# Kernel tuning notes

Hardware: AMD Instinct MI355X
Metric: run time of the kernel (lower is better)

Reference implementation:

```python
import jax, jax.numpy as jnp
import numpy as np

EPS = 1e-6
NH, D_NOPE, D_ROPE, DV = 16, 128, 64, 128
DQK = D_NOPE + D_ROPE  # 192
KV_LORA = 512
Q_LORA = 1536
TOP_K, N_GROUP, TOPK_GROUP, N_EXP = 2, 4, 2, 8
INTER = 768
SCALING = DQK ** -0.5  # rope_scaling is None -> no yarn mscale
RSF = 2.5  # routed_scaling_factor


def rms_norm(x, w):
    v = jnp.mean(jnp.square(x), axis=-1, keepdims=True)
    return x * jax.lax.rsqrt(v + EPS) * w


def rotate_half(x):
    x1, x2 = jnp.split(x, 2, axis=-1)
    return jnp.concatenate([-x2, x1], axis=-1)


def interleave(x):
    # view(b,h,s,d//2,2).transpose(4,3).reshape(b,h,s,d): evens then odds
    b, h, s, d = x.shape
    return x.reshape(b, h, s, d // 2, 2).swapaxes(-1, -2).reshape(b, h, s, d)


def mlp(x, gw, uw, dw):
    return (jax.nn.silu(x @ gw.T) * (x @ uw.T)) @ dw.T


def setup_inputs() -> dict:
    key = jax.random.key(0)
    ks = jax.random.split(key, 16)
    B, S, H = 2, 1024, 2048
    sd = 0.02

    def p(k, shape):
        return jax.random.normal(k, shape, jnp.float32) * sd

    # standard RoPE cos/sin table
    inv_freq = 1.0 / (10000.0 ** (jnp.arange(0, D_ROPE, 2, dtype=jnp.float32) / D_ROPE))
    pos = jnp.arange(S, dtype=jnp.float32)
    freqs = pos[:, None] * inv_freq[None, :]
    emb = jnp.concatenate([freqs, freqs], axis=-1)  # [S, D_ROPE]
    cos = jnp.broadcast_to(jnp.cos(emb)[None], (B, S, D_ROPE))
    sin = jnp.broadcast_to(jnp.sin(emb)[None], (B, S, D_ROPE))

    return dict(
        hidden_states=jax.random.normal(ks[0], (B, S, H), jnp.float32),
        cos=cos,
        sin=sin,
        ln1_w=jnp.ones((H,), jnp.float32),
        q_a_w=p(ks[1], (Q_LORA, H)),
        q_a_ln_w=jnp.ones((Q_LORA,), jnp.float32),
        q_b_w=p(ks[2], (NH * DQK, Q_LORA)),
        kv_a_w=p(ks[3], (KV_LORA + D_ROPE, H)),
        kv_a_ln_w=jnp.ones((KV_LORA,), jnp.float32),
        kv_b_w=p(ks[4], (NH * (D_NOPE + DV), KV_LORA)),
        o_w=p(ks[5], (H, NH * DV)),
        ln2_w=jnp.ones((H,), jnp.float32),
        router_w=p(ks[6], (N_EXP, H)),
        router_bias=jnp.zeros((N_EXP,), jnp.float32),
        gate_w=p(ks[7], (N_EXP, INTER, H)),
        up_w=p(ks[8], (N_EXP, INTER, H)),
        down_w=p(ks[9], (N_EXP, H, INTER)),
        sh_gate_w=p(ks[10], (INTER, H)),
        sh_up_w=p(ks[11], (INTER, H)),
        sh_down_w=p(ks[12], (H, INTER)),
    )


def reference(hidden_states, cos, sin, ln1_w, q_a_w, q_a_ln_w, q_b_w, kv_a_w,
              kv_a_ln_w, kv_b_w, o_w, ln2_w, router_w, router_bias,
              gate_w, up_w, down_w, sh_gate_w, sh_up_w, sh_down_w):
    B, S, H = hidden_states.shape
    # ----- input_layernorm + MLA attention -----
    resid = hidden_states
    x = rms_norm(hidden_states, ln1_w)

    q = rms_norm(x @ q_a_w.T, q_a_ln_w) @ q_b_w.T       # [B,S,NH*DQK]
    q = q.reshape(B, S, NH, DQK).transpose(0, 2, 1, 3)   # [B,NH,S,DQK]
    q_pass, q_rot = q[..., :D_NOPE], q[..., D_NOPE:]

    ckv = x @ kv_a_w.T                                   # [B,S,KV_LORA+D_ROPE]
    k_pass_c, k_rot = ckv[..., :KV_LORA], ckv[..., KV_LORA:]
    kv = rms_norm(k_pass_c, kv_a_ln_w) @ kv_b_w.T        # [B,S,NH*(D_NOPE+DV)]
    kv = kv.reshape(B, S, NH, D_NOPE + DV).transpose(0, 2, 1, 3)
    k_pass, v = kv[..., :D_NOPE], kv[..., D_NOPE:]

    k_rot = k_rot.reshape(B, 1, S, D_ROPE)
    c = cos[:, None]  # [B,1,S,D_ROPE]
    s_ = sin[:, None]
    q_rot = interleave(q_rot)
    k_rot = interleave(k_rot)
    q_rot = q_rot * c + rotate_half(q_rot) * s_
    k_rot = k_rot * c + rotate_half(k_rot) * s_
    k_rot = jnp.broadcast_to(k_rot, (B, NH, S, D_ROPE))

    qs = jnp.concatenate([q_pass, q_rot], axis=-1)       # [B,NH,S,DQK]
    ks = jnp.concatenate([k_pass, k_rot], axis=-1)

    scores = jnp.einsum('bhqd,bhkd->bhqk', qs, ks) * SCALING
    causal = jnp.tril(jnp.ones((S, S), dtype=bool))
    scores = jnp.where(causal, scores, -jnp.inf)
    probs = jax.nn.softmax(scores, axis=-1)
    attn = jnp.einsum('bhqk,bhkd->bhqd', probs, v)
    attn = attn.transpose(0, 2, 1, 3).reshape(B, S, NH * DV)
    x = resid + attn @ o_w.T

    # ----- post_attention_layernorm + MoE -----
    resid = x
    h = rms_norm(x, ln2_w)
    t = h.reshape(-1, H)

    # router (fp32)
    scores_r = jax.nn.sigmoid(t.astype(jnp.float32) @ router_w.T.astype(jnp.float32))
    sc = scores_r + router_bias[None, :]
    gs = sc.reshape(-1, N_GROUP, N_EXP // N_GROUP)
    group_scores = jax.lax.top_k(gs, 2)[0].sum(-1)          # [T,G]
    gidx = jax.lax.top_k(group_scores, TOPK_GROUP)[1]
    gmask = jax.nn.one_hot(gidx, N_GROUP).sum(1)            # [T,G]
    emask = jnp.repeat(gmask, N_EXP // N_GROUP, axis=-1)    # [T,E]
    masked = jnp.where(emask > 0, sc, 0.0)
    idx = jax.lax.top_k(masked, TOP_K)[1]                   # [T,k]
    w = jnp.take_along_axis(scores_r, idx, axis=-1)
    w = w / (w.sum(-1, keepdims=True) + 1e-20) * RSF

    # routed experts: dense-all-experts compute, then routed-weight combine
    gate_h = jnp.einsum('td,eid->tei', t, gate_w)
    up_h = jnp.einsum('td,eid->tei', t, up_w)
    eo = jnp.einsum('tei,edi->ted', jax.nn.silu(gate_h) * up_h, down_w)
    dense_w = (jax.nn.one_hot(idx, N_EXP) * w[..., None]).sum(1)  # [T,E]
    moe_out = jnp.einsum('ted,te->td', eo, dense_w).reshape(B, S, H)

    shared = mlp(h, sh_gate_w, sh_up_w, sh_down_w)
    return resid + moe_out + shared
```

## Files before the change

kernel.cpp:

```cpp
#include <hip/hip_runtime.h>

typedef float f4 __attribute__((ext_vector_type(4)));
typedef float f32x4 __attribute__((ext_vector_type(4)));
typedef unsigned short us8 __attribute__((ext_vector_type(8)));
typedef __bf16 bf8 __attribute__((ext_vector_type(8)));

static constexpr int B_ = 2, S_ = 1024, H_ = 2048, T_ = B_ * S_;
static constexpr int NH_ = 16, DN_ = 128, DR_ = 64, DV_ = 128, DQK_ = 192;
static constexpr int KVL_ = 512, QL_ = 1536, INTER_ = 768, NEXP_ = 8, NE9_ = 9;
static constexpr int QKA_ = 2176;
static constexpr float SCALING_ = 0.07216878364870322f;
static constexpr float EPS_ = 1e-6f;

__device__ __forceinline__ unsigned short f2bf(float f) {
    unsigned u = __float_as_uint(f);
    u += 0x7fffu + ((u >> 16) & 1u);
    return (unsigned short)(u >> 16);
}
__device__ __forceinline__ float bf2f(unsigned short h) {
    return __uint_as_float(((unsigned)h) << 16);
}
__device__ __forceinline__ us8 pack8(f4 a, f4 b) {
    us8 r;
    r[0] = f2bf(a[0]); r[1] = f2bf(a[1]); r[2] = f2bf(a[2]); r[3] = f2bf(a[3]);
    r[4] = f2bf(b[0]); r[5] = f2bf(b[1]); r[6] = f2bf(b[2]); r[7] = f2bf(b[3]);
    return r;
}

__device__ __forceinline__ void gload16(const unsigned short* g, unsigned short* lds) {
    __builtin_amdgcn_global_load_lds(
        (const __attribute__((address_space(1))) void*)g,
        (__attribute__((address_space(3))) void*)lds, 16, 0, 0);
}

template <int MODE>
__global__ __launch_bounds__(256) void gemm2(
    const unsigned short* __restrict__ A, const unsigned short* __restrict__ Bw,
    float* __restrict__ Cf, unsigned short* __restrict__ Cb,
    const float* __restrict__ add,
    const int* __restrict__ cnt, const int* __restrict__ off,
    const int* __restrict__ idxl, const float* __restrict__ wl,
    int M, int N, int K, int ldA, long sB)
{
    constexpr int BM = 128, BN = 128, BK = 32;
    __shared__ __align__(16) unsigned short As[5][BM * BK];
    __shared__ __align__(16) unsigned short Bs[5][BN * BK];
    const int tid = threadIdx.x, lane = tid & 63, wv = tid >> 6;
    const int wm = (wv >> 1) * 64, wn = (wv & 1) * 64;

    const int nb = gridDim.x * gridDim.y;
    const int lin = blockIdx.y * gridDim.x + blockIdx.x;
    const int swz = (lin & 7) * (nb >> 3) + (lin >> 3);
    const int bx = swz % gridDim.x;
    const int by = swz / gridDim.x;
    const int m0 = bx * BM, n0 = by * BN;

    int mcnt = M, obase = 0;
    if constexpr (MODE != 0) {
        mcnt = cnt[blockIdx.z];
        if (m0 >= mcnt) return;
        obase = off[blockIdx.z];
    }

    const int srow = tid >> 2, scol = (tid & 3) * 8;
    long aoff0, aoff1;
    if constexpr (MODE == 1) {
        const int e = blockIdx.z;
        int r0 = m0 + srow, r1 = r0 + 64;
        int t0 = idxl[(long)e * T_ + (r0 < mcnt ? r0 : mcnt - 1)];
        int t1 = idxl[(long)e * T_ + (r1 < mcnt ? r1 : mcnt - 1)];
        aoff0 = (long)t0 * ldA + scol;
        aoff1 = (long)t1 * ldA + scol;
    } else if constexpr (MODE == 2) {
        aoff0 = (long)(obase + m0 + srow) * ldA + scol;
        aoff1 = aoff0 + 64L * ldA;
    } else {
        aoff0 = (long)(m0 + srow) * ldA + scol;
        aoff1 = aoff0 + 64L * ldA;
    }
    long boff0 = (long)blockIdx.z * sB + (long)(n0 + srow) * K + scol;
    long boff1 = boff0 + 64L * K;

    f32x4 acc[4][4];
#pragma unroll
    for (int m = 0; m < 4; m++)
#pragma unroll
        for (int n = 0; n < 4; n++) acc[m][n] = f32x4{0.f, 0.f, 0.f, 0.f};

    const int fr = lane & 15, ko = (lane >> 4) * 8;

    auto stage = [&](int buf, int k0) {
        gload16(A + aoff0 + k0, &As[buf][wv * 512]);
        gload16(A + aoff1 + k0, &As[buf][2048 + wv * 512]);
        gload16(Bw + boff0 + k0, &Bs[buf][wv * 512]);
        gload16(Bw + boff1 + k0, &Bs[buf][2048 + wv * 512]);
    };
    auto compute = [&](int buf) {
        __builtin_amdgcn_s_setprio(1);
        bf8 af[4], bfv[4];
#pragma unroll
        for (int m = 0; m < 4; m++) af[m] = *(const bf8*)&As[buf][(wm + m * 16 + fr) * 32 + ko];
#pragma unroll
        for (int n = 0; n < 4; n++) bfv[n] = *(const bf8*)&Bs[buf][(wn + n * 16 + fr) * 32 + ko];
#pragma unroll
        for (int m = 0; m < 4; m++)
#pragma unroll
            for (int n = 0; n < 4; n++)
                acc[m][n] = __builtin_amdgcn_mfma_f32_16x16x32_bf16(af[m], bfv[n], acc[m][n], 0, 0, 0);
        __builtin_amdgcn_s_setprio(0);
    };

    const int nt = K / BK;
    stage(0, 0);
    stage(1, BK);
    stage(2, 2 * BK);
    stage(3, 3 * BK);
    for (int t = 0; t < nt; t++) {
        if (t + 3 < nt)      asm volatile("s_waitcnt vmcnt(12)" ::: "memory");
        else if (t + 2 < nt) asm volatile("s_waitcnt vmcnt(8)" ::: "memory");
        else if (t + 1 < nt) asm volatile("s_waitcnt vmcnt(4)" ::: "memory");
        else                 asm volatile("s_waitcnt vmcnt(0)" ::: "memory");
        __builtin_amdgcn_s_barrier();
        if (t + 4 < nt) stage((t + 4) % 5, (t + 4) * BK);
        compute(t % 5);
    }

#pragma unroll
    for (int m = 0; m < 4; m++) {
#pragma unroll
        for (int n = 0; n < 4; n++) {
#pragma unroll
            for (int i = 0; i < 4; i++) {
                int row = wm + m * 16 + (lane >> 4) * 4 + i;
                int col = n0 + wn + n * 16 + (lane & 15);
                float v = acc[m][n][i];
                if constexpr (MODE == 0) {
                    long idx = (long)(m0 + row) * N + col;
                    if (Cb)       Cb[idx] = f2bf(v);
                    else if (add) Cf[idx] = v + add[idx];
                    else          Cf[idx] = v;
                } else if constexpr (MODE == 1) {
                    if (m0 + row < mcnt)
                        Cb[(long)(obase + m0 + row) * N + col] = f2bf(v);
                } else {
                    if (m0 + row < mcnt) {
                        int e = blockIdx.z;
                        int tok = idxl[(long)e * T_ + m0 + row];
                        float w = wl[(long)e * T_ + m0 + row];
                        atomicAdd(&Cf[(long)tok * N + col], w * v);
                    }
                }
            }
        }
    }
}

__global__ __launch_bounds__(256) void fa_k(
    const unsigned short* __restrict__ qs, const unsigned short* __restrict__ ks,
    const unsigned short* __restrict__ vt, unsigned short* __restrict__ ab)
{
    constexpr int KB = 64;
    const int q0 = blockIdx.x * 64;
    const int bh = blockIdx.y;
    const int b = bh >> 4, h = bh & 15;
    const int tid = threadIdx.x, lane = tid & 63, wv = tid >> 6;
    const int fr = lane & 15, lg = lane >> 4;
    const int ko = lg * 8;

    __shared__ __align__(16) unsigned short Kl[KB][200];
    __shared__ __align__(16) unsigned short Vl[128][72];
    __shared__ __align__(16) unsigned short Pl[4][16][72];

    const unsigned short* qp = qs + ((long)bh * S_ + q0 + wv * 16 + fr) * DQK_ + ko;
    bf8 qf[6];
#pragma unroll
    for (int s = 0; s < 6; s++) qf[s] = *(const bf8*)(qp + s * 32);

    f32x4 o[8];
#pragma unroll
    for (int n = 0; n < 8; n++) o[n] = f32x4{0.f, 0.f, 0.f, 0.f};
    float mrow[4] = {-3e38f, -3e38f, -3e38f, -3e38f};
    float lrow[4] = {0.f, 0.f, 0.f, 0.f};

    const int nt = q0 / KB + 1;

    const unsigned short* kg = ks + ((long)bh * S_ + (tid >> 2)) * DQK_ + (tid & 3) * 48;
    const unsigned short* vg = vt + ((long)bh * DV_ + (tid >> 1)) * S_ + (tid & 1) * 32;

    us8 krg[6], vrg[4];
#pragma unroll
    for (int j = 0; j < 6; j++) krg[j] = *(const us8*)(kg + j * 8);
#pragma unroll
    for (int j = 0; j < 4; j++) vrg[j] = *(const us8*)(vg + j * 8);

    for (int t = 0; t < nt; t++) {
        __syncthreads();
        {
            int r = tid >> 2, c = (tid & 3) * 48;
#pragma unroll
            for (int j = 0; j < 6; j++) *(us8*)&Kl[r][c + j * 8] = krg[j];
            int dv = tid >> 1, c2 = (tid & 1) * 32;
#pragma unroll
            for (int j = 0; j < 4; j++) *(us8*)&Vl[dv][c2 + j * 8] = vrg[j];
        }
        __syncthreads();
        if (t + 1 < nt) {
            long kof = (long)(t + 1) * KB;
#pragma unroll
            for (int j = 0; j < 6; j++) krg[j] = *(const us8*)(kg + kof * DQK_ + j * 8);
#pragma unroll
            for (int j = 0; j < 4; j++) vrg[j] = *(const us8*)(vg + kof + j * 8);
        }
        f32x4 ps[4];
#pragma unroll
        for (int ct = 0; ct < 4; ct++) {
            f32x4 a = f32x4{0.f, 0.f, 0.f, 0.f};
#pragma unroll
            for (int s = 0; s < 6; s++) {
                bf8 kf = *(const bf8*)&Kl[ct * 16 + fr][s * 32 + ko];
                a = __builtin_amdgcn_mfma_f32_16x16x32_bf16(qf[s], kf, a, 0, 0, 0);
            }
            ps[ct] = a;
        }
        const int kv0 = t * KB;
        const bool diag = (kv0 == q0);
#pragma unroll
        for (int ct = 0; ct < 4; ct++)
#pragma unroll
            for (int i = 0; i < 4; i++) {
                float v = ps[ct][i] * SCALING_;
                if (diag && (kv0 + ct * 16 + fr) > (q0 + wv * 16 + lg * 4 + i)) v = -3e38f;
                ps[ct][i] = v;
            }
        float scl[4];
#pragma unroll
        for (int i = 0; i < 4; i++) {
            float v = fmaxf(fmaxf(ps[0][i], ps[1][i]), fmaxf(ps[2][i], ps[3][i]));
#pragma unroll
            for (int x = 8; x; x >>= 1) v = fmaxf(v, __shfl_xor(v, x, 16));
            float mn = fmaxf(mrow[i], v);
            scl[i] = __expf(mrow[i] - mn);
            mrow[i] = mn;
        }
        float tsum[4] = {0.f, 0.f, 0.f, 0.f};
#pragma unroll
        for (int ct = 0; ct < 4; ct++)
#pragma unroll
            for (int i = 0; i < 4; i++) {
                float e = __expf(ps[ct][i] - mrow[i]);
                tsum[i] += e;
                Pl[wv][lg * 4 + i][ct * 16 + fr] = f2bf(e);
            }
#pragma unroll
        for (int i = 0; i < 4; i++) {
            float v = tsum[i];
#pragma unroll
            for (int x = 8; x; x >>= 1) v += __shfl_xor(v, x, 16);
            lrow[i] = lrow[i] * scl[i] + v;
        }
#pragma unroll
        for (int n = 0; n < 8; n++)
#pragma unroll
            for (int i = 0; i < 4; i++) o[n][i] *= scl[i];
        bf8 pf[2];
#pragma unroll
        for (int ksl = 0; ksl < 2; ksl++)
            pf[ksl] = *(const bf8*)&Pl[wv][fr][ksl * 32 + ko];
#pragma unroll
        for (int n = 0; n < 8; n++)
#pragma unroll
            for (int ksl = 0; ksl < 2; ksl++) {
                bf8 vf = *(const bf8*)&Vl[n * 16 + fr][ksl * 32 + ko];
                o[n] = __builtin_amdgcn_mfma_f32_16x16x32_bf16(pf[ksl], vf, o[n], 0, 0, 0);
            }
    }
#pragma unroll
    for (int i = 0; i < 4; i++) {
        float inv = 1.f / lrow[i];
        long rbase = ((long)b * S_ + q0 + wv * 16 + lg * 4 + i) * H_ + h * DV_;
#pragma unroll
        for (int n = 0; n < 8; n++)
            ab[rbase + n * 16 + fr] = f2bf(o[n][i] * inv);
    }
}

__global__ __launch_bounds__(256) void cvt_k(
    const float* __restrict__ s, unsigned short* __restrict__ d, long n)
{
    long i = ((long)blockIdx.x * 256 + threadIdx.x) * 8;
    if (i < n) {
        f4 a = *(const f4*)(s + i);
        f4 b = *(const f4*)(s + i + 4);
        *(us8*)(d + i) = pack8(a, b);
    }
}

__global__ __launch_bounds__(256) void cvt_qka_k(
    const float* __restrict__ qa, const float* __restrict__ kva,
    unsigned short* __restrict__ d)
{
    long i = ((long)blockIdx.x * 256 + threadIdx.x) * 8;
    long row = i >> 11, col = i & 2047;
    us8 o;
    if (row < QL_) {
        const float* s = qa + row * H_ + col;
        o = pack8(*(const f4*)s, *(const f4*)(s + 4));
    } else if (row < QL_ + 576) {
        const float* s = kva + (row - QL_) * H_ + col;
        o = pack8(*(const f4*)s, *(const f4*)(s + 4));
    } else {
        o = us8{0, 0, 0, 0, 0, 0, 0, 0};
    }
    *(us8*)(d + i) = o;
}

__global__ __launch_bounds__(256) void cvt_cat9_k(
    const float* __restrict__ g, const float* __restrict__ u,
    const float* __restrict__ sg, const float* __restrict__ su,
    unsigned short* __restrict__ d)
{
    long ii = ((long)blockIdx.x * 256 + threadIdx.x) * 8;
    int e = blockIdx.y;
    long row = ii >> 11, col = ii & 2047;
    const float* src;
    if (row < INTER_)
        src = (e < 8) ? (g + ((long)e * INTER_ + row) * H_ + col) : (sg + row * H_ + col);
    else
        src = (e < 8) ? (u + ((long)e * INTER_ + row - INTER_) * H_ + col)
                      : (su + (row - INTER_) * H_ + col);
    *(us8*)(d + (long)e * (2 * INTER_) * H_ + ii) = pack8(*(const f4*)src, *(const f4*)(src + 4));
}

__global__ __launch_bounds__(256) void rmsnorm_f2b(
    const float* __restrict__ in, const float* __restrict__ w,
    unsigned short* __restrict__ ob, float* __restrict__ of)
{
    const long base = (long)blockIdx.x * H_;
    const int c = threadIdx.x * 8;
    f4 v0 = *(const f4*)(in + base + c);
    f4 v1 = *(const f4*)(in + base + c + 4);
    float ss = v0[0] * v0[0] + v0[1] * v0[1] + v0[2] * v0[2] + v0[3] * v0[3]
             + v1[0] * v1[0] + v1[1] * v1[1] + v1[2] * v1[2] + v1[3] * v1[3];
#pragma unroll
    for (int o = 32; o; o >>= 1) ss += __shfl_down(ss, o);
    __shared__ float red[4];
    if ((threadIdx.x & 63) == 0) red[threadIdx.x >> 6] = ss;
    __syncthreads();
    float r = rsqrtf((red[0] + red[1] + red[2] + red[3]) / H_ + EPS_);
    f4 w0 = *(const f4*)(w + c);
    f4 w1 = *(const f4*)(w + c + 4);
    f4 a, b;
#pragma unroll
    for (int j = 0; j < 4; j++) { a[j] = v0[j] * r * w0[j]; b[j] = v1[j] * r * w1[j]; }
    *(us8*)(ob + base + c) = pack8(a, b);
    if (of) {
        *(f4*)(of + base + c) = a;
        *(f4*)(of + base + c + 4) = b;
    }
}

__global__ __launch_bounds__(256) void rmsnorm_b2b(
    const unsigned short* __restrict__ in, const float* __restrict__ w,
    unsigned short* __restrict__ out, int cols, int istride, int ostride)
{
    const long ib = (long)blockIdx.x * istride;
    const long ob = (long)blockIdx.x * ostride;
    const int nu = cols >> 3;
    float ss = 0.f;
    for (int u = threadIdx.x; u < nu; u += 256) {
        us8 v = *(const us8*)(in + ib + u * 8);
#pragma unroll
        for (int j = 0; j < 8; j++) { float f = bf2f(v[j]); ss += f * f; }
    }
#pragma unroll
    for (int o = 32; o; o >>= 1) ss += __shfl_down(ss, o);
    __shared__ float red[4];
    if ((threadIdx.x & 63) == 0) red[threadIdx.x >> 6] = ss;
    __syncthreads();
    float r = rsqrtf((red[0] + red[1] + red[2] + red[3]) / cols + EPS_);
    for (int u = threadIdx.x; u < nu; u += 256) {
        us8 v = *(const us8*)(in + ib + u * 8);
        f4 w0 = *(const f4*)(w + u * 8);
        f4 w1 = *(const f4*)(w + u * 8 + 4);
        us8 o;
#pragma unroll
        for (int j = 0; j < 4; j++) o[j] = f2bf(bf2f(v[j]) * r * w0[j]);
#pragma unroll
        for (int j = 0; j < 4; j++) o[4 + j] = f2bf(bf2f(v[4 + j]) * r * w1[j]);
        *(us8*)(out + ob + u * 8) = o;
    }
}

__global__ __launch_bounds__(64) void rope_q_k(
    const unsigned short* __restrict__ q, const float* __restrict__ cs,
    const float* __restrict__ sn, unsigned short* __restrict__ qs)
{
    int t = blockIdx.x;
    int h = t & 15;
    int bs = t >> 4;
    int s = bs & (S_ - 1);
    int b = bs >> 10;
    const unsigned short* qrow = q + (long)bs * (NH_ * DQK_) + h * DQK_;
    unsigned short* orow = qs + ((long)(b * NH_ + h) * S_ + s) * DQK_;
    int l = threadIdx.x;
    orow[l] = qrow[l];
    orow[l + 64] = qrow[l + 64];
    int j = l & 31;
    float x0 = bf2f(qrow[DN_ + 2 * j]), x1 = bf2f(qrow[DN_ + 2 * j + 1]);
    float c = cs[(long)bs * DR_ + j], si = sn[(long)bs * DR_ + j];
    if (l < 32) orow[DN_ + j] = f2bf(x0 * c - x1 * si);
    else        orow[DN_ + 32 + j] = f2bf(x1 * c + x0 * si);
}

__global__ __launch_bounds__(64) void rope_k_k(
    const unsigned short* __restrict__ qkab, const float* __restrict__ cs,
    const float* __restrict__ sn, unsigned short* __restrict__ ks)
{
    int bs = blockIdx.x;
    int s = bs & (S_ - 1);
    int b = bs >> 10;
    const unsigned short* kr = qkab + (long)bs * QKA_ + QL_ + KVL_;
    int l = threadIdx.x;
    int j = l & 31;
    float x0 = bf2f(kr[2 * j]), x1 = bf2f(kr[2 * j + 1]);
    float c = cs[(long)bs * DR_ + j], si = sn[(long)bs * DR_ + j];
    float val = (l < 32) ? (x0 * c - x1 * si) : (x1 * c + x0 * si);
    int off = (l < 32) ? (DN_ + j) : (DN_ + 32 + j);
    unsigned short bv = f2bf(val);
    for (int h = 0; h < NH_; h++)
        ks[((long)(b * NH_ + h) * S_ + s) * DQK_ + off] = bv;
}

__global__ __launch_bounds__(128) void kpass_k(
    const unsigned short* __restrict__ kv, unsigned short* __restrict__ ks)
{
    int t = blockIdx.x;
    int h = t & 15;
    int bs = t >> 4;
    int s = bs & (S_ - 1);
    int b = bs >> 10;
    ks[((long)(b * NH_ + h) * S_ + s) * DQK_ + threadIdx.x] = kv[(long)t * 256 + threadIdx.x];
}

__global__ __launch_bounds__(256) void vt_k(
    const unsigned short* __restrict__ kv, unsigned short* __restrict__ vt)
{
    __shared__ unsigned short tile[64][DV_ + 8];
    int s0 = blockIdx.x * 64;
    int bh = blockIdx.y;
    int b = bh >> 4, h = bh & 15;
#pragma unroll
    for (int it = 0; it < 4; it++) {
        int idx = it * 256 + threadIdx.x;
        int sl = idx >> 4, du = idx & 15;
        *(us8*)&tile[sl][du * 8] =
            *(const us8*)(kv + ((long)(b * S_ + s0 + sl) * NH_ + h) * 256 + DN_ + du * 8);
    }
    __syncthreads();
#pragma unroll
    for (int it = 0; it < 4; it++) {
        int idx = it * 256 + threadIdx.x;
        int d = idx >> 3, su = idx & 7;
        us8 o;
#pragma unroll
        for (int j = 0; j < 8; j++) o[j] = tile[su * 8 + j][d];
        *(us8*)(vt + ((long)bh * DV_ + d) * S_ + s0 + su * 8) = o;
    }
}

__global__ void zero9_k(int* __restrict__ cnt)
{
    if (threadIdx.x < NE9_) cnt[threadIdx.x] = (threadIdx.x == 8) ? T_ : 0;
}

__global__ void offs_k(const int* __restrict__ cnt, int* __restrict__ off)
{
    if (threadIdx.x == 0) {
        int a = 0;
        for (int e = 0; e < NE9_; e++) { off[e] = a; a += cnt[e]; }
    }
}

__global__ __launch_bounds__(64) void router_k(
    const float* __restrict__ h, const float* __restrict__ rw,
    const float* __restrict__ rb, int* __restrict__ cnt,
    int* __restrict__ idxl, float* __restrict__ wl)
{
    int t = blockIdx.x;
    int l = threadIdx.x;
    const float* hr = h + (long)t * H_;
    float pe[8] = {0, 0, 0, 0, 0, 0, 0, 0};
    for (int k = l; k < H_; k += 64) {
        float hv = hr[k];
#pragma unroll
        for (int e = 0; e < 8; e++) pe[e] += hv * rw[e * H_ + k];
    }
#pragma unroll
    for (int e = 0; e < 8; e++)
        for (int o = 32; o; o >>= 1) pe[e] += __shfl_down(pe[e], o);
    if (l == 0) {
        float sr[8], sc[8];
#pragma unroll
        for (int e = 0; e < 8; e++) {
            sr[e] = 1.f / (1.f + __expf(-pe[e]));
            sc[e] = sr[e] + rb[e];
        }
        float gs[4];
        for (int g = 0; g < 4; g++) gs[g] = sc[2 * g] + sc[2 * g + 1];
        int g0 = 0;
        for (int g = 1; g < 4; g++) if (gs[g] > gs[g0]) g0 = g;
        int g1 = -1;
        for (int g = 0; g < 4; g++) {
            if (g == g0) continue;
            if (g1 < 0 || gs[g] > gs[g1]) g1 = g;
        }
        int i0 = -1, i1 = -1;
        for (int e = 0; e < 8; e++) {
            int g = e >> 1;
            if (g != g0 && g != g1) continue;
            if (i0 < 0 || sc[e] > sc[i0]) i0 = e;
        }
        for (int e = 0; e < 8; e++) {
            int g = e >> 1;
            if (g != g0 && g != g1) continue;
            if (e == i0) continue;
            if (i1 < 0 || sc[e] > sc[i1]) i1 = e;
        }
        float w0 = sr[i0], w1 = sr[i1];
        float inv = 2.5f / (w0 + w1 + 1e-20f);
        int p0 = atomicAdd(&cnt[i0], 1);
        idxl[i0 * T_ + p0] = t;
        wl[i0 * T_ + p0] = w0 * inv;
        int p1 = atomicAdd(&cnt[i1], 1);
        idxl[i1 * T_ + p1] = t;
        wl[i1 * T_ + p1] = w1 * inv;
        idxl[8 * T_ + t] = t;
        wl[8 * T_ + t] = 1.0f;
    }
}

__global__ __launch_bounds__(256) void silugu_k(
    const unsigned short* __restrict__ gu, unsigned short* __restrict__ act)
{
    long idx = (long)blockIdx.x * 256 + threadIdx.x;
    int r = (int)(idx / 96);
    int c = (int)(idx - (long)r * 96) * 8;
    us8 g8 = *(const us8*)(gu + (long)r * (2 * INTER_) + c);
    us8 u8 = *(const us8*)(gu + (long)r * (2 * INTER_) + INTER_ + c);
    us8 o;
#pragma unroll
    for (int j = 0; j < 8; j++) {
        float g = bf2f(g8[j]);
        o[j] = f2bf(g / (1.f + __expf(-g)) * bf2f(u8[j]));
    }
    *(us8*)(act + (long)r * INTER_ + c) = o;
}

extern "C" void kernel_launch(void* const* d_in, const int* in_sizes, int n_in,
                              void* d_out, int out_size, void* d_ws, size_t ws_size,
                              hipStream_t stream)
{
    const float* hidden = (const float*)d_in[0];
    const float* cosb   = (const float*)d_in[1];
    const float* sinb   = (const float*)d_in[2];
    const float* ln1w   = (const float*)d_in[3];
    const float* qaw    = (const float*)d_in[4];
    const float* qalnw  = (const float*)d_in[5];
    const float* qbw    = (const float*)d_in[6];
    const float* kvaw   = (const float*)d_in[7];
    const float* kvalnw = (const float*)d_in[8];
    const float* kvbw   = (const float*)d_in[9];
    const float* ow     = (const float*)d_in[10];
    const float* ln2w   = (const float*)d_in[11];
    const float* rw     = (const float*)d_in[12];
    const float* rb     = (const float*)d_in[13];
    const float* gw     = (const float*)d_in[14];
    const float* uw     = (const float*)d_in[15];
    const float* dwn    = (const float*)d_in[16];
    const float* sgw    = (const float*)d_in[17];
    const float* suw    = (const float*)d_in[18];
    const float* sdw    = (const float*)d_in[19];
    float* out = (float*)d_out;
    (void)in_sizes; (void)n_in; (void)out_size; (void)ws_size;

    char* ws = (char*)d_ws;
    const size_t MB = 1u << 20;
    unsigned short* qkawb = (unsigned short*)(ws + 0 * MB);
    unsigned short* qbwb  = (unsigned short*)(ws + 9 * MB);
    unsigned short* kvbwb = (unsigned short*)(ws + 18 * MB);
    unsigned short* owb   = (unsigned short*)(ws + 22 * MB);
    unsigned short* xb    = (unsigned short*)(ws + 30 * MB);
    unsigned short* qkab  = (unsigned short*)(ws + 38 * MB);
    unsigned short* qb16  = (unsigned short*)(ws + 47 * MB);
    unsigned short* ckvnb = (unsigned short*)(ws + 59 * MB);
    unsigned short* kvb   = (unsigned short*)(ws + 61 * MB);
    unsigned short* qs    = (unsigned short*)(ws + 77 * MB);
    unsigned short* ks    = (unsigned short*)(ws + 89 * MB);
    unsigned short* vt    = (unsigned short*)(ws + 30 * MB);
    unsigned short* ab    = (unsigned short*)(ws + 38 * MB);
    float* hbuf = (float*)(ws + 0 * MB);
    unsigned short* actm = (unsigned short*)(ws + 0 * MB);
    unsigned short* hb16 = (unsigned short*)(ws + 16 * MB);
    int*   cnt  = (int*)(ws + 24 * MB);
    int*   offb = (int*)(ws + 24 * MB + 256);
    int*   idxl = (int*)(ws + 24 * MB + 512);
    float* wl   = (float*)(ws + 24 * MB + 512 + 9 * T_ * 4);
    unsigned short* guwb = (unsigned short*)(ws + 25 * MB);
    unsigned short* dwnb = (unsigned short*)(ws + 25 * MB);
    unsigned short* gu   = (unsigned short*)(ws + 79 * MB);

    cvt_qka_k<<<(QKA_ * H_) / 2048, 256, 0, stream>>>(qaw, kvaw, qkawb);
    cvt_k<<<(NH_ * DQK_ * QL_) / 2048, 256, 0, stream>>>(qbw, qbwb, (long)NH_ * DQK_ * QL_);
    cvt_k<<<(NH_ * 256 * KVL_) / 2048, 256, 0, stream>>>(kvbw, kvbwb, (long)NH_ * 256 * KVL_);
    cvt_k<<<(H_ * H_) / 2048, 256, 0, stream>>>(ow, owb, (long)H_ * H_);

    rmsnorm_f2b<<<T_, 256, 0, stream>>>(hidden, ln1w, xb, nullptr);

    gemm2<0><<<dim3(T_ / 128, QKA_ / 128, 1), 256, 0, stream>>>(
        xb, qkawb, nullptr, qkab, nullptr, nullptr, nullptr, nullptr, nullptr,
        T_, QKA_, H_, H_, 0);
    rmsnorm_b2b<<<T_, 256, 0, stream>>>(qkab, qalnw, qkab, QL_, QKA_, QKA_);
    gemm2<0><<<dim3(T_ / 128, (NH_ * DQK_) / 128, 1), 256, 0, stream>>>(
        qkab, qbwb, nullptr, qb16, nullptr, nullptr, nullptr, nullptr, nullptr,
        T_, NH_ * DQK_, QL_, QKA_, 0);
    rmsnorm_b2b<<<T_, 256, 0, stream>>>(qkab + QL_, kvalnw, ckvnb, KVL_, QKA_, KVL_);
    gemm2<0><<<dim3(T_ / 128, (NH_ * 256) / 128, 1), 256, 0, stream>>>(
        ckvnb, kvbwb, nullptr, kvb, nullptr, nullptr, nullptr, nullptr, nullptr,
        T_, NH_ * 256, KVL_, KVL_, 0);

    rope_q_k<<<T_ * NH_, 64, 0, stream>>>(qb16, cosb, sinb, qs);
    rope_k_k<<<T_, 64, 0, stream>>>(qkab, cosb, sinb, ks);
    kpass_k<<<T_ * NH_, 128, 0, stream>>>(kvb, ks);
    vt_k<<<dim3(S_ / 64, B_ * NH_), 256, 0, stream>>>(kvb, vt);

    fa_k<<<dim3(S_ / 64, B_ * NH_), 256, 0, stream>>>(qs, ks, vt, ab);

    gemm2<0><<<dim3(T_ / 128, H_ / 128, 1), 256, 0, stream>>>(
        ab, owb, out, nullptr, hidden, nullptr, nullptr, nullptr, nullptr,
        T_, H_, H_, H_, 0);

    rmsnorm_f2b<<<T_, 256, 0, stream>>>(out, ln2w, hb16, hbuf);
    zero9_k<<<1, 64, 0, stream>>>(cnt);
    router_k<<<T_, 64, 0, stream>>>(hbuf, rw, rb, cnt, idxl, wl);
    offs_k<<<1, 64, 0, stream>>>(cnt, offb);

    cvt_cat9_k<<<dim3((2 * INTER_ * H_) / 2048, NE9_), 256, 0, stream>>>(gw, uw, sgw, suw, guwb);
    gemm2<1><<<dim3(T_ / 128, (2 * INTER_) / 128, NE9_), 256, 0, stream>>>(
        hb16, guwb, nullptr, gu, nullptr, cnt, offb, idxl, nullptr,
        T_, 2 * INTER_, H_, H_, (long)(2 * INTER_) * H_);
    silugu_k<<<(3 * T_ * 96) / 256, 256, 0, stream>>>(gu, actm);
    cvt_k<<<(NEXP_ * H_ * INTER_) / 2048, 256, 0, stream>>>(dwn, dwnb, (long)NEXP_ * H_ * INTER_);
    cvt_k<<<(H_ * INTER_) / 2048, 256, 0, stream>>>(sdw, dwnb + (long)NEXP_ * H_ * INTER_, (long)H_ * INTER_);
    gemm2<2><<<dim3(T_ / 128, H_ / 128, NE9_), 256, 0, stream>>>(
        actm, dwnb, out, nullptr, nullptr, cnt, offb, idxl, wl,
        T_, H_, INTER_, INTER_, (long)H_ * INTER_);
}
```

Measured before the change: 600.5 us.

## Double BK to 64 with XOR-swizzled LDS and double buffering in GEMM

Raises the GEMM K-tile from 32 to 64, replaces the 5-stage prefetch ring with a 2-buffer double-buffered pipeline, and XOR-swizzles LDS columns to avoid bank conflicts on fragment reads. The aim is to halve loop iterations and barriers per K and to cut LDS read conflicts. In exchange there is an extra barrier per iteration and a shallower prefetch depth, so global-load latency may be hidden less well.

Measured after the change: 534.4 us. 11.0% less time.

```diff
diff --git a/kernel.cpp b/kernel.cpp
--- a/kernel.cpp
+++ b/kernel.cpp
@@ -42,9 +42,9 @@
     const int* __restrict__ idxl, const float* __restrict__ wl,
     int M, int N, int K, int ldA, long sB)
 {
-    constexpr int BM = 128, BN = 128, BK = 32;
-    __shared__ __align__(16) unsigned short As[5][BM * BK];
-    __shared__ __align__(16) unsigned short Bs[5][BN * BK];
+    constexpr int BM = 128, BN = 128, BK = 64;
+    __shared__ __align__(16) unsigned short As[2][BM * BK];
+    __shared__ __align__(16) unsigned short Bs[2][BN * BK];
     const int tid = threadIdx.x, lane = tid & 63, wv = tid >> 6;
     const int wm = (wv >> 1) * 64, wn = (wv & 1) * 64;
 
@@ -62,24 +62,22 @@
         obase = off[blockIdx.z];
     }
 
-    const int srow = tid >> 2, scol = (tid & 3) * 8;
-    long aoff0, aoff1;
-    if constexpr (MODE == 1) {
-        const int e = blockIdx.z;
-        int r0 = m0 + srow, r1 = r0 + 64;
-        int t0 = idxl[(long)e * T_ + (r0 < mcnt ? r0 : mcnt - 1)];
-        int t1 = idxl[(long)e * T_ + (r1 < mcnt ? r1 : mcnt - 1)];
-        aoff0 = (long)t0 * ldA + scol;
-        aoff1 = (long)t1 * ldA + scol;
-    } else if constexpr (MODE == 2) {
-        aoff0 = (long)(obase + m0 + srow) * ldA + scol;
-        aoff1 = aoff0 + 64L * ldA;
-    } else {
-        aoff0 = (long)(m0 + srow) * ldA + scol;
-        aoff1 = aoff0 + 64L * ldA;
-    }
-    long boff0 = (long)blockIdx.z * sB + (long)(n0 + srow) * K + scol;
-    long boff1 = boff0 + 64L * K;
+    const int srow = tid >> 3;
+    const int scol = (((tid & 7) ^ (srow & 7)) * 8);
+    long aoff[4], boff[4];
+#pragma unroll
+    for (int s = 0; s < 4; s++) {
+        int r = m0 + s * 32 + srow;
+        if constexpr (MODE == 1) {
+            int rc = (r < mcnt) ? r : mcnt - 1;
+            aoff[s] = (long)idxl[(long)blockIdx.z * T_ + rc] * ldA + scol;
+        } else if constexpr (MODE == 2) {
+            aoff[s] = (long)(obase + r) * ldA + scol;
+        } else {
+            aoff[s] = (long)r * ldA + scol;
+        }
+        boff[s] = (long)blockIdx.z * sB + (long)(n0 + s * 32 + srow) * K + scol;
+    }
 
     f32x4 acc[4][4];
 #pragma unroll
@@ -87,42 +85,56 @@
 #pragma unroll
         for (int n = 0; n < 4; n++) acc[m][n] = f32x4{0.f, 0.f, 0.f, 0.f};
 
-    const int fr = lane & 15, ko = (lane >> 4) * 8;
+    const int fr = lane & 15, lg = lane >> 4;
+    const int xr = fr & 7;
 
     auto stage = [&](int buf, int k0) {
-        gload16(A + aoff0 + k0, &As[buf][wv * 512]);
-        gload16(A + aoff1 + k0, &As[buf][2048 + wv * 512]);
-        gload16(Bw + boff0 + k0, &Bs[buf][wv * 512]);
-        gload16(Bw + boff1 + k0, &Bs[buf][2048 + wv * 512]);
+#pragma unroll
+        for (int s = 0; s < 4; s++)
+            gload16(A + aoff[s] + k0, &As[buf][s * 2048 + wv * 512]);
+#pragma unroll
+        for (int s = 0; s < 4; s++)
+            gload16(Bw + boff[s] + k0, &Bs[buf][s * 2048 + wv * 512]);
     };
     auto compute = [&](int buf) {
         __builtin_amdgcn_s_setprio(1);
-        bf8 af[4], bfv[4];
-#pragma unroll
-        for (int m = 0; m < 4; m++) af[m] = *(const bf8*)&As[buf][(wm + m * 16 + fr) * 32 + ko];
-#pragma unroll
-        for (int n = 0; n < 4; n++) bfv[n] = *(const bf8*)&Bs[buf][(wn + n * 16 + fr) * 32 + ko];
+        bf8 af[4][2], bfv[4][2];
+#pragma unroll
+        for (int m = 0; m < 4; m++) {
+            int R = wm + m * 16 + fr;
+#pragma unroll
+            for (int ks = 0; ks < 2; ks++)
+                af[m][ks] = *(const bf8*)&As[buf][R * 64 + ((ks * 4 + lg) ^ xr) * 8];
+        }
+#pragma unroll
+        for (int n = 0; n < 4; n++) {
+            int R = wn + n * 16 + fr;
+#pragma unroll
+            for (int ks = 0; ks < 2; ks++)
+                bfv[n][ks] = *(const bf8*)&Bs[buf][R * 64 + ((ks * 4 + lg) ^ xr) * 8];
+        }
 #pragma unroll
         for (int m = 0; m < 4; m++)
 #pragma unroll
-            for (int n = 0; n < 4; n++)
-                acc[m][n] = __builtin_amdgcn_mfma_f32_16x16x32_bf16(af[m], bfv[n], acc[m][n], 0, 0, 0);
+            for (int n = 0; n < 4; n++) {
+                acc[m][n] = __builtin_amdgcn_mfma_f32_16x16x32_bf16(af[m][0], bfv[n][0], acc[m][n], 0, 0, 0);
+                acc[m][n] = __builtin_amdgcn_mfma_f32_16x16x32_bf16(af[m][1], bfv[n][1], acc[m][n], 0, 0, 0);
+            }
         __builtin_amdgcn_s_setprio(0);
     };
 
     const int nt = K / BK;
     stage(0, 0);
-    stage(1, BK);
-    stage(2, 2 * BK);
-    stage(3, 3 * BK);
     for (int t = 0; t < nt; t++) {
-        if (t + 3 < nt)      asm volatile("s_waitcnt vmcnt(12)" ::: "memory");
-        else if (t + 2 < nt) asm volatile("s_waitcnt vmcnt(8)" ::: "memory");
-        else if (t + 1 < nt) asm volatile("s_waitcnt vmcnt(4)" ::: "memory");
-        else                 asm volatile("s_waitcnt vmcnt(0)" ::: "memory");
+        if (t + 1 < nt) {
+            stage((t & 1) ^ 1, (t + 1) * BK);
+            asm volatile("s_waitcnt vmcnt(8)" ::: "memory");
+        } else {
+            asm volatile("s_waitcnt vmcnt(0)" ::: "memory");
+        }
         __builtin_amdgcn_s_barrier();
-        if (t + 4 < nt) stage((t + 4) % 5, (t + 4) * BK);
-        compute(t % 5);
+        compute(t & 1);
+        __builtin_amdgcn_s_barrier();
     }
 
 #pragma unroll
```
